# Kernel tuning notes

Measured on AMD Instinct MI355X. Metric: run time of the kernel, lower is better.

## Reference

```python
import jax, jax.numpy as jnp
import numpy as np

# Standard SMPL kinematic tree (child -> parent); root's entry unused.
PARENTS = np.array([0, 0, 0, 0, 1, 2, 3, 4, 5, 6, 7, 8, 9, 9, 9, 12, 13, 14, 16, 17, 18, 19, 20, 21], dtype=np.int32)
N_JOINTS = 24


def _rodrigues(r):
    # r: [..., 3] axis-angle -> [..., 3, 3] rotation matrices.
    # Original adds N(0,1e-8) noise to avoid div-by-zero; we use a deterministic eps.
    theta = jnp.linalg.norm(r, axis=-1, keepdims=True) + 1e-8
    rh = r / theta
    cos = jnp.cos(theta)[..., None]
    sin = jnp.sin(theta)[..., None]
    z = jnp.zeros_like(rh[..., 0])
    K = jnp.stack([z, -rh[..., 2], rh[..., 1],
                   rh[..., 2], z, -rh[..., 0],
                   -rh[..., 1], rh[..., 0], z], axis=-1).reshape(r.shape[:-1] + (3, 3))
    outer = rh[..., :, None] * rh[..., None, :]
    eye = jnp.eye(3, dtype=r.dtype)
    return cos * eye + (1.0 - cos) * outer + sin * K


def setup_inputs() -> dict:
    key = jax.random.key(0)
    ks = jax.random.split(key, 7)
    N, V, J, B = 512, 6890, 24, 10
    beta = jax.random.normal(ks[0], (N, B), dtype=jnp.float32)
    pose = jax.random.normal(ks[1], (N, J * 3), dtype=jnp.float32)
    v_template = jax.random.normal(ks[2], (V, 3), dtype=jnp.float32)
    shapedirs = jax.random.normal(ks[3], (V, 3, B), dtype=jnp.float32) * 0.03
    posedirs = jax.random.normal(ks[4], (V, 3, (J - 1) * 9), dtype=jnp.float32) * 0.01
    J_regressor = jax.random.uniform(ks[5], (J, V), dtype=jnp.float32)
    J_regressor = J_regressor / jnp.sum(J_regressor, axis=1, keepdims=True)  # NonNegUnitSum(axis=1)
    weights = jax.random.uniform(ks[6], (V, J), dtype=jnp.float32)
    weights = weights / jnp.sum(weights, axis=1, keepdims=True)  # NonNegUnitSum(axis=1)
    return {"beta": beta, "pose": pose, "v_template": v_template, "shapedirs": shapedirs,
            "posedirs": posedirs, "J_regressor": J_regressor, "weights": weights}


def reference(beta, pose, v_template, shapedirs, posedirs, J_regressor, weights):
    N = beta.shape[0]
    dt = beta.dtype
    # Shape blendshapes: [N,V,3]
    v_shaped = jnp.einsum('nb,vcb->nvc', beta, shapedirs) + v_template
    # Joint locations: [N,J,3]
    J_loc = jnp.einsum('jv,nvc->njc', J_regressor, v_shaped)
    # Per-joint rotations: [N,24,3,3]
    R = _rodrigues(pose.reshape(N, N_JOINTS, 3))
    # Pose blendshapes
    lrotmin = (R[:, 1:] - jnp.eye(3, dtype=dt)).reshape(N, (N_JOINTS - 1) * 9)
    v_posed = v_shaped + jnp.einsum('np,vcp->nvc', lrotmin, posedirs)
    # Kinematic chain of 4x4 transforms
    bottom = jnp.broadcast_to(jnp.array([0.0, 0.0, 0.0, 1.0], dtype=dt), (N, 1, 4))

    def make_T(Rm, t):  # [N,3,3], [N,3] -> [N,4,4]
        return jnp.concatenate([jnp.concatenate([Rm, t[..., None]], axis=-1), bottom], axis=-2)

    G = [make_T(R[:, 0], J_loc[:, 0])]
    for i in range(1, N_JOINTS):
        p = int(PARENTS[i])
        G.append(jnp.matmul(G[p], make_T(R[:, i], J_loc[:, i] - J_loc[:, p])))
    G = jnp.stack(G, axis=1)  # [N,24,4,4]
    # Remove rest-pose joint translation: G[...,:,3] -= G @ [J,0]
    Jh = jnp.concatenate([J_loc, jnp.zeros_like(J_loc[..., :1])], axis=-1)  # [N,24,4]
    RJ = jnp.einsum('njab,njb->nja', G, Jh)
    G = G - jnp.pad(RJ[..., None], ((0, 0), (0, 0), (0, 0), (3, 0)))
    # Linear blend skinning: per-vertex blended transform [N,V,4,4]
    T = jnp.einsum('njab,vj->nvab', G, weights)
    vh = jnp.concatenate([v_posed, jnp.ones_like(v_posed[..., :1])], axis=-1)  # [N,V,4]
    v = jnp.einsum('nvab,nvb->nva', T, vh)
    return v[..., :3]
```

## Files before the change

kernel.cpp:

```cpp
#include <hip/hip_runtime.h>

#define V_CNT 6890
#define N_B 512
#define NP 207
#define KPAD 224
#define RTOT 20670
#define RPAD 20736
#define PREP_BLKS 2268
#define JS1_BLKS 384
#define W_BLKS 27

typedef unsigned short ushort_t;
typedef __attribute__((ext_vector_type(4))) float f32x4;
typedef __attribute__((ext_vector_type(8))) short s16x8;
typedef __attribute__((ext_vector_type(2))) float f32x2;

#define O_PART 0u
#define O_G2   65536u
#define O_A    655360u
#define O_W    917504u
#define O_B    1441792u
#define O_PB   10747904u

__device__ __constant__ int PAR[24] = {0,0,0,0,1,2,3,4,5,6,7,8,9,9,9,12,13,14,16,17,18,19,20,21};
__device__ __constant__ int LVL[36] = {
    1, 2, 3,-1,   4, 5, 6,-1,   7, 8, 9,-1,
   10,11,12,13,  14,-1,-1,-1,  15,16,17,-1,
   18,19,-1,-1,  20,21,-1,-1,  22,23,-1,-1};

__device__ __forceinline__ ushort_t f2bf(float f) {
    union { float f; unsigned u; } x; x.f = f;
    unsigned u = x.u + 0x7fffu + ((x.u >> 16) & 1u);
    return (ushort_t)(u >> 16);
}
__device__ __forceinline__ float bf2f(ushort_t h) {
    union { unsigned u; float f; } x; x.u = ((unsigned)h) << 16;
    return x.f;
}

__global__ __launch_bounds__(256) void k_pre(const float* __restrict__ pdirs,
                                             const float* __restrict__ sdirs,
                                             const float* __restrict__ vtemp,
                                             const float* __restrict__ jreg,
                                             const float* __restrict__ wts,
                                             ushort_t* __restrict__ Bm,
                                             float* __restrict__ part,
                                             ushort_t* __restrict__ Wp) {
    int b = blockIdx.x;
    int tid = threadIdx.x;
    if (b < PREP_BLKS) {
        int g = b * 256 + tid;
        int r = g / 28;
        int k0 = (g - r * 28) * 8;
        s16x8 pk;
        if (r < RTOT) {
            const float* pr = pdirs + (size_t)r * NP;
            const float* sr = sdirs + (size_t)r * 10;
#pragma unroll
            for (int i = 0; i < 8; i++) {
                int k = k0 + i;
                float v = 0.f;
                if (k < NP) v = pr[k];
                else if (k < 217) v = sr[k - NP];
                pk[i] = (short)f2bf(v);
            }
        } else {
#pragma unroll
            for (int i = 0; i < 8; i++) pk[i] = 0;
        }
        *(s16x8*)(Bm + (size_t)r * KPAD + k0) = pk;
    } else if (b < PREP_BLKS + JS1_BLKS) {
        int b2 = b - PREP_BLKS;
        int ch = b2 & 15;
        int j = b2 >> 4;
        int v0 = ch * 432;
        int vend = v0 + 432; if (vend > V_CNT) vend = V_CNT;
        float acc[33];
#pragma unroll
        for (int i = 0; i < 33; i++) acc[i] = 0.f;
        for (int v = v0 + tid; v < vend; v += 256) {
            float r = jreg[j * V_CNT + v];
            const float* sd = sdirs + v * 30;
#pragma unroll
            for (int i = 0; i < 30; i++) acc[i] += r * sd[i];
            acc[30] += r * vtemp[v * 3 + 0];
            acc[31] += r * vtemp[v * 3 + 1];
            acc[32] += r * vtemp[v * 3 + 2];
        }
#pragma unroll
        for (int off = 32; off > 0; off >>= 1) {
#pragma unroll
            for (int i = 0; i < 33; i++) acc[i] += __shfl_down(acc[i], off);
        }
        __shared__ float red[4][33];
        int w = tid >> 6, lane = tid & 63;
        if (lane == 0) {
#pragma unroll
            for (int i = 0; i < 33; i++) red[w][i] = acc[i];
        }
        __syncthreads();
        if (tid < 33) {
            float s = red[0][tid] + red[1][tid] + red[2][tid] + red[3][tid];
            part[b2 * 33 + tid] = s;
        }
    } else {
        int v = (b - PREP_BLKS - JS1_BLKS) * 256 + tid;
        ushort_t o[32];
        if (v < V_CNT) {
            const float* wr = wts + v * 24;
#pragma unroll
            for (int j = 0; j < 24; j++) o[j] = f2bf(wr[j]);
        } else {
#pragma unroll
            for (int j = 0; j < 24; j++) o[j] = 0;
        }
#pragma unroll
        for (int j = 24; j < 32; j++) o[j] = 0;
#pragma unroll
        for (int q = 0; q < 4; q++)
            *(s16x8*)(Wp + (size_t)v * 32 + q * 8) = *(s16x8*)&o[q * 8];
    }
}

__global__ __launch_bounds__(128) void k_chain(const float* __restrict__ beta,
                                               const float* __restrict__ pose,
                                               const float* __restrict__ part,
                                               ushort_t* __restrict__ G2,
                                               ushort_t* __restrict__ Am) {
    __shared__ float JSl[720];
    __shared__ float JTl[72];
    __shared__ float Rl[2][24][9];
    __shared__ float Jl[2][24][3];
    __shared__ float Tm[2][24][16];
    __shared__ float G[2][24][16];
    __shared__ float Gp[2][24][12];
    int tid = threadIdx.x;

    for (int t = tid; t < 792; t += 128) {
        int j = t / 33, i = t - j * 33;
        float s = 0.f;
#pragma unroll
        for (int c = 0; c < 16; c++) s += part[(j * 16 + c) * 33 + i];
        if (i < 30) JSl[j * 30 + i] = s;
        else        JTl[j * 3 + (i - 30)] = s;
    }
    __syncthreads();

    int sub = tid >> 6, lane = tid & 63;
    int n = blockIdx.x * 2 + sub;

    if (lane < 24) {
        int t = lane;
        float x = pose[n * 72 + t * 3 + 0];
        float y = pose[n * 72 + t * 3 + 1];
        float z = pose[n * 72 + t * 3 + 2];
        float th = sqrtf(x * x + y * y + z * z) + 1e-8f;
        float inv = 1.f / th;
        float rx = x * inv, ry = y * inv, rz = z * inv;
        float c = cosf(th), s = sinf(th), omc = 1.f - c;
        Rl[sub][t][0] = c + omc * rx * rx;
        Rl[sub][t][1] = omc * rx * ry - s * rz;
        Rl[sub][t][2] = omc * rx * rz + s * ry;
        Rl[sub][t][3] = omc * ry * rx + s * rz;
        Rl[sub][t][4] = c + omc * ry * ry;
        Rl[sub][t][5] = omc * ry * rz - s * rx;
        Rl[sub][t][6] = omc * rz * rx - s * ry;
        Rl[sub][t][7] = omc * rz * ry + s * rx;
        Rl[sub][t][8] = c + omc * rz * rz;
#pragma unroll
        for (int cc = 0; cc < 3; cc++) {
            float a = JTl[t * 3 + cc];
#pragma unroll
            for (int b = 0; b < 10; b++) a += beta[n * 10 + b] * JSl[(t * 3 + cc) * 10 + b];
            Jl[sub][t][cc] = a;
        }
    }
    __syncthreads();
    if (lane < 24) {
        int t = lane;
        int p = PAR[t];
        float tx, ty, tz;
        if (t == 0) { tx = Jl[sub][0][0]; ty = Jl[sub][0][1]; tz = Jl[sub][0][2]; }
        else { tx = Jl[sub][t][0] - Jl[sub][p][0]; ty = Jl[sub][t][1] - Jl[sub][p][1]; tz = Jl[sub][t][2] - Jl[sub][p][2]; }
        Tm[sub][t][0] = Rl[sub][t][0]; Tm[sub][t][1] = Rl[sub][t][1]; Tm[sub][t][2]  = Rl[sub][t][2]; Tm[sub][t][3]  = tx;
        Tm[sub][t][4] = Rl[sub][t][3]; Tm[sub][t][5] = Rl[sub][t][4]; Tm[sub][t][6]  = Rl[sub][t][5]; Tm[sub][t][7]  = ty;
        Tm[sub][t][8] = Rl[sub][t][6]; Tm[sub][t][9] = Rl[sub][t][7]; Tm[sub][t][10] = Rl[sub][t][8]; Tm[sub][t][11] = tz;
        Tm[sub][t][12] = 0.f; Tm[sub][t][13] = 0.f; Tm[sub][t][14] = 0.f; Tm[sub][t][15] = 1.f;
    }
    __syncthreads();
    if (lane < 16) G[sub][0][lane] = Tm[sub][0][lane];
    __syncthreads();
#pragma unroll
    for (int p9 = 0; p9 < 9; p9++) {
        int slot = lane >> 4, el = lane & 15;
        int j = LVL[p9 * 4 + slot];
        if (j >= 0) {
            int par = PAR[j];
            int a = el >> 2, bb = el & 3;
            float s = G[sub][par][a * 4 + 0] * Tm[sub][j][0 * 4 + bb]
                    + G[sub][par][a * 4 + 1] * Tm[sub][j][1 * 4 + bb]
                    + G[sub][par][a * 4 + 2] * Tm[sub][j][2 * 4 + bb]
                    + G[sub][par][a * 4 + 3] * Tm[sub][j][3 * 4 + bb];
            G[sub][j][el] = s;
        }
        __syncthreads();
    }
    if (lane < 24) {
        int t = lane;
        float jx = Jl[sub][t][0], jy = Jl[sub][t][1], jz = Jl[sub][t][2];
#pragma unroll
        for (int a = 0; a < 3; a++) {
            float g0 = G[sub][t][a * 4 + 0], g1 = G[sub][t][a * 4 + 1];
            float g2 = G[sub][t][a * 4 + 2], g3 = G[sub][t][a * 4 + 3];
            Gp[sub][t][a * 4 + 0] = g0;
            Gp[sub][t][a * 4 + 1] = g1;
            Gp[sub][t][a * 4 + 2] = g2;
            Gp[sub][t][a * 4 + 3] = g3 - (g0 * jx + g1 * jy + g2 * jz);
        }
    }
    __syncthreads();
    {
        int quad = lane >> 4, lm = lane & 15;
        s16x8 pk;
#pragma unroll
        for (int jj = 0; jj < 8; jj++) {
            int joint = quad * 8 + jj;
            float val = (joint < 24 && lm < 12) ? Gp[sub][joint][lm] : 0.f;
            pk[jj] = (short)f2bf(val);
        }
        *(s16x8*)(G2 + (size_t)n * 512 + lane * 8) = pk;
    }
    for (int idx = lane; idx < KPAD; idx += 64) {
        float val;
        if (idx < NP) {
            int j = 1 + idx / 9;
            int e = idx - (j - 1) * 9;
            float d = (e == 0 || e == 4 || e == 8) ? 1.f : 0.f;
            val = Rl[sub][j][e] - d;
        } else if (idx < 217) {
            val = beta[n * 10 + (idx - NP)];
        } else val = 0.f;
        Am[n * KPAD + idx] = f2bf(val);
    }
}

__global__ __launch_bounds__(256) void k_gemm(const ushort_t* __restrict__ A,
                                              const ushort_t* __restrict__ B,
                                              const float* __restrict__ vtemp,
                                              ushort_t* __restrict__ C) {
    __shared__ __align__(16) ushort_t a_lds[128 * 40];
    __shared__ __align__(16) ushort_t b_lds[128 * 40];
    int tid = threadIdx.x;
    int rblk = blockIdx.x * 128;
    int n0 = blockIdx.y * 128;
    int w = tid >> 6, lane = tid & 63;
    int quad = lane >> 4, lm = lane & 15;
    int m0w = (w >> 1) * 64, r0w = (w & 1) * 64;

    f32x4 acc[4][4];
#pragma unroll
    for (int a = 0; a < 4; a++)
#pragma unroll
        for (int b = 0; b < 4; b++) acc[a][b] = (f32x4)0.f;

    int srow = tid >> 1, koff = (tid & 1) * 16;
    const ushort_t* ag = A + (size_t)(n0 + srow) * KPAD + koff;
    const ushort_t* bg = B + (size_t)(rblk + srow) * KPAD + koff;

#pragma unroll 1
    for (int kc = 0; kc < 7; kc++) {
        s16x8 av0 = *(const s16x8*)(ag + kc * 32);
        s16x8 av1 = *(const s16x8*)(ag + kc * 32 + 8);
        s16x8 bv0 = *(const s16x8*)(bg + kc * 32);
        s16x8 bv1 = *(const s16x8*)(bg + kc * 32 + 8);
        __syncthreads();
        *(s16x8*)&a_lds[srow * 40 + koff] = av0;
        *(s16x8*)&a_lds[srow * 40 + koff + 8] = av1;
        *(s16x8*)&b_lds[srow * 40 + koff] = bv0;
        *(s16x8*)&b_lds[srow * 40 + koff + 8] = bv1;
        __syncthreads();
        s16x8 af[4], bf[4];
#pragma unroll
        for (int mt = 0; mt < 4; mt++)
            af[mt] = *(const s16x8*)&a_lds[(m0w + mt * 16 + lm) * 40 + quad * 8];
#pragma unroll
        for (int rt = 0; rt < 4; rt++)
            bf[rt] = *(const s16x8*)&b_lds[(r0w + rt * 16 + lm) * 40 + quad * 8];
#pragma unroll
        for (int mt = 0; mt < 4; mt++)
#pragma unroll
            for (int rt = 0; rt < 4; rt++)
                acc[mt][rt] = __builtin_amdgcn_mfma_f32_16x16x32_bf16(af[mt], bf[rt], acc[mt][rt], 0, 0, 0);
    }
#pragma unroll
    for (int mt = 0; mt < 4; mt++) {
#pragma unroll
        for (int rt = 0; rt < 4; rt++) {
            int col = rblk + r0w + rt * 16 + lm;
            float vt = (col < RTOT) ? vtemp[col] : 0.f;
#pragma unroll
            for (int i = 0; i < 4; i++) {
                int row = n0 + m0w + mt * 16 + quad * 4 + i;
                C[(size_t)row * RPAD + col] = f2bf(acc[mt][rt][i] + vt);
            }
        }
    }
}

__global__ __launch_bounds__(256) void k_lbs(const ushort_t* __restrict__ Wp,
                                             const ushort_t* __restrict__ G2,
                                             const ushort_t* __restrict__ pb,
                                             float* __restrict__ out) {
    __shared__ float T[4][64][19];
    __shared__ float ost[4][192];
    int tid = threadIdx.x, w = tid >> 6, lane = tid & 63;
    int quad = lane >> 4, lm = lane & 15;
    int v0 = blockIdx.x * 256;
    int n = blockIdx.y * 4 + w;

    s16x8 bfr = *(const s16x8*)(G2 + (size_t)n * 512 + lane * 8);
    const ushort_t* pbn = pb + (size_t)n * RPAD;

#pragma unroll 1
    for (int s = 0; s < 4; s++) {
        int vs = v0 + s * 64;
        const ushort_t* pp = pbn + (vs + lane) * 3;
        float px = bf2f(pp[0]), py = bf2f(pp[1]), pz = bf2f(pp[2]);

        f32x4 acc[4];
#pragma unroll
        for (int mt = 0; mt < 4; mt++) {
            s16x8 af = *(const s16x8*)(Wp + (size_t)(vs + mt * 16 + lm) * 32 + quad * 8);
            acc[mt] = __builtin_amdgcn_mfma_f32_16x16x32_bf16(af, bfr, (f32x4)0.f, 0, 0, 0);
        }
#pragma unroll
        for (int mt = 0; mt < 4; mt++)
#pragma unroll
            for (int i = 0; i < 4; i++)
                T[w][mt * 16 + quad * 4 + i][lm] = acc[mt][i];

        const float* Tr = &T[w][lane][0];
        float o0 = Tr[3]  + Tr[0] * px + Tr[1] * py + Tr[2]  * pz;
        float o1 = Tr[7]  + Tr[4] * px + Tr[5] * py + Tr[6]  * pz;
        float o2 = Tr[11] + Tr[8] * px + Tr[9] * py + Tr[10] * pz;
        ost[w][lane * 3 + 0] = o0;
        ost[w][lane * 3 + 1] = o1;
        ost[w][lane * 3 + 2] = o2;

        int cnt = V_CNT - vs; if (cnt > 64) cnt = 64;
        if (cnt > 0) {
            int nh = (cnt * 3) >> 1;
            float* obase = out + ((size_t)n * V_CNT + vs) * 3;
            for (int j2 = lane; j2 < nh; j2 += 64)
                *(f32x2*)(obase + j2 * 2) = *(const f32x2*)&ost[w][j2 * 2];
        }
    }
}

extern "C" void kernel_launch(void* const* d_in, const int* in_sizes, int n_in,
                              void* d_out, int out_size, void* d_ws, size_t ws_size,
                              hipStream_t stream) {
    const float* beta  = (const float*)d_in[0];
    const float* pose  = (const float*)d_in[1];
    const float* vtemp = (const float*)d_in[2];
    const float* sdirs = (const float*)d_in[3];
    const float* pdirs = (const float*)d_in[4];
    const float* jreg  = (const float*)d_in[5];
    const float* wts   = (const float*)d_in[6];
    char* ws = (char*)d_ws;
    float*    ws_part = (float*)(ws + O_PART);
    ushort_t* ws_G2   = (ushort_t*)(ws + O_G2);
    ushort_t* ws_A    = (ushort_t*)(ws + O_A);
    ushort_t* ws_W    = (ushort_t*)(ws + O_W);
    ushort_t* ws_B    = (ushort_t*)(ws + O_B);
    ushort_t* ws_pb   = (ushort_t*)(ws + O_PB);
    float* out = (float*)d_out;

    k_pre<<<dim3(PREP_BLKS + JS1_BLKS + W_BLKS), dim3(256), 0, stream>>>(
        pdirs, sdirs, vtemp, jreg, wts, ws_B, ws_part, ws_W);
    k_chain<<<dim3(N_B / 2), dim3(128), 0, stream>>>(beta, pose, ws_part, ws_G2, ws_A);
    k_gemm<<<dim3(RPAD / 128, N_B / 128), dim3(256), 0, stream>>>(ws_A, ws_B, vtemp, ws_pb);
    k_lbs<<<dim3(27, N_B / 4), dim3(256), 0, stream>>>(ws_W, ws_G2, ws_pb, out);
}
```

Measured before the change: 148.1 us.

## Fuse blendshape GEMM with skinning and pre-swizzle operands into MFMA fragment layout

The separate GEMM kernel that wrote posed vertices to a bf16 global buffer and the skinning kernel that read them back are merged into one kernel. Each wave keeps its GEMM tile in LDS and applies the blended joint transforms directly. A and B are pre-swizzled into MFMA fragment order so the GEMM loads fragments straight from global with register double-buffering and no LDS staging. This removes a roughly 21 MB intermediate round trip and one launch, at the cost of higher register and LDS use per block and more, smaller blocks. The joint-regressor partial reduction is also halved to 8 chunks.

New measurement: 142.0 us. 1.04x faster.

```diff
diff --git a/kernel.cpp b/kernel.cpp
--- a/kernel.cpp
+++ b/kernel.cpp
@@ -7,7 +7,7 @@
 #define RTOT 20670
 #define RPAD 20736
 #define PREP_BLKS 2268
-#define JS1_BLKS 384
+#define JS1_BLKS 192
 #define W_BLKS 27
 
 typedef unsigned short ushort_t;
@@ -20,7 +20,6 @@
 #define O_A    655360u
 #define O_W    917504u
 #define O_B    1441792u
-#define O_PB   10747904u
 
 __device__ __constant__ int PAR[24] = {0,0,0,0,1,2,3,4,5,6,7,8,9,9,9,12,13,14,16,17,18,19,20,21};
 __device__ __constant__ int LVL[36] = {
@@ -43,15 +42,20 @@
                                              const float* __restrict__ vtemp,
                                              const float* __restrict__ jreg,
                                              const float* __restrict__ wts,
-                                             ushort_t* __restrict__ Bm,
+                                             ushort_t* __restrict__ Bswz,
                                              float* __restrict__ part,
                                              ushort_t* __restrict__ Wp) {
     int b = blockIdx.x;
     int tid = threadIdx.x;
     if (b < PREP_BLKS) {
         int g = b * 256 + tid;
-        int r = g / 28;
-        int k0 = (g - r * 28) * 8;
+        int rtile = g / 448;
+        int rem = g - rtile * 448;
+        int kc = rem >> 6;
+        int lane = rem & 63;
+        int quad = lane >> 4, lm = lane & 15;
+        int r = rtile * 16 + lm;
+        int k0 = kc * 32 + quad * 8;
         s16x8 pk;
         if (r < RTOT) {
             const float* pr = pdirs + (size_t)r * NP;
@@ -68,13 +72,13 @@
 #pragma unroll
             for (int i = 0; i < 8; i++) pk[i] = 0;
         }
-        *(s16x8*)(Bm + (size_t)r * KPAD + k0) = pk;
+        *(s16x8*)(Bswz + (size_t)g * 8) = pk;
     } else if (b < PREP_BLKS + JS1_BLKS) {
         int b2 = b - PREP_BLKS;
-        int ch = b2 & 15;
-        int j = b2 >> 4;
-        int v0 = ch * 432;
-        int vend = v0 + 432; if (vend > V_CNT) vend = V_CNT;
+        int ch = b2 & 7;
+        int j = b2 >> 3;
+        int v0 = ch * 862;
+        int vend = v0 + 862; if (vend > V_CNT) vend = V_CNT;
         float acc[33];
 #pragma unroll
         for (int i = 0; i < 33; i++) acc[i] = 0.f;
@@ -126,7 +130,7 @@
                                                const float* __restrict__ pose,
                                                const float* __restrict__ part,
                                                ushort_t* __restrict__ G2,
-                                               ushort_t* __restrict__ Am) {
+                                               ushort_t* __restrict__ Aswz) {
     __shared__ float JSl[720];
     __shared__ float JTl[72];
     __shared__ float Rl[2][24][9];
@@ -140,7 +144,7 @@
         int j = t / 33, i = t - j * 33;
         float s = 0.f;
 #pragma unroll
-        for (int c = 0; c < 16; c++) s += part[(j * 16 + c) * 33 + i];
+        for (int c = 0; c < 8; c++) s += part[(j * 8 + c) * 33 + i];
         if (i < 30) JSl[j * 30 + i] = s;
         else        JTl[j * 3 + (i - 30)] = s;
     }
@@ -230,129 +234,138 @@
         }
         *(s16x8*)(G2 + (size_t)n * 512 + lane * 8) = pk;
     }
-    for (int idx = lane; idx < KPAD; idx += 64) {
-        float val;
-        if (idx < NP) {
-            int j = 1 + idx / 9;
-            int e = idx - (j - 1) * 9;
-            float d = (e == 0 || e == 4 || e == 8) ? 1.f : 0.f;
-            val = Rl[sub][j][e] - d;
-        } else if (idx < 217) {
-            val = beta[n * 10 + (idx - NP)];
-        } else val = 0.f;
-        Am[n * KPAD + idx] = f2bf(val);
-    }
-}
-
-__global__ __launch_bounds__(256) void k_gemm(const ushort_t* __restrict__ A,
-                                              const ushort_t* __restrict__ B,
-                                              const float* __restrict__ vtemp,
-                                              ushort_t* __restrict__ C) {
-    __shared__ __align__(16) ushort_t a_lds[128 * 40];
-    __shared__ __align__(16) ushort_t b_lds[128 * 40];
-    int tid = threadIdx.x;
-    int rblk = blockIdx.x * 128;
-    int n0 = blockIdx.y * 128;
-    int w = tid >> 6, lane = tid & 63;
-    int quad = lane >> 4, lm = lane & 15;
-    int m0w = (w >> 1) * 64, r0w = (w & 1) * 64;
-
-    f32x4 acc[4][4];
-#pragma unroll
-    for (int a = 0; a < 4; a++)
-#pragma unroll
-        for (int b = 0; b < 4; b++) acc[a][b] = (f32x4)0.f;
-
-    int srow = tid >> 1, koff = (tid & 1) * 16;
-    const ushort_t* ag = A + (size_t)(n0 + srow) * KPAD + koff;
-    const ushort_t* bg = B + (size_t)(rblk + srow) * KPAD + koff;
-
-#pragma unroll 1
-    for (int kc = 0; kc < 7; kc++) {
-        s16x8 av0 = *(const s16x8*)(ag + kc * 32);
-        s16x8 av1 = *(const s16x8*)(ag + kc * 32 + 8);
-        s16x8 bv0 = *(const s16x8*)(bg + kc * 32);
-        s16x8 bv1 = *(const s16x8*)(bg + kc * 32 + 8);
-        __syncthreads();
-        *(s16x8*)&a_lds[srow * 40 + koff] = av0;
-        *(s16x8*)&a_lds[srow * 40 + koff + 8] = av1;
-        *(s16x8*)&b_lds[srow * 40 + koff] = bv0;
-        *(s16x8*)&b_lds[srow * 40 + koff + 8] = bv1;
-        __syncthreads();
-        s16x8 af[4], bf[4];
-#pragma unroll
-        for (int mt = 0; mt < 4; mt++)
-            af[mt] = *(const s16x8*)&a_lds[(m0w + mt * 16 + lm) * 40 + quad * 8];
-#pragma unroll
-        for (int rt = 0; rt < 4; rt++)
-            bf[rt] = *(const s16x8*)&b_lds[(r0w + rt * 16 + lm) * 40 + quad * 8];
-#pragma unroll
-        for (int mt = 0; mt < 4; mt++)
-#pragma unroll
-            for (int rt = 0; rt < 4; rt++)
-                acc[mt][rt] = __builtin_amdgcn_mfma_f32_16x16x32_bf16(af[mt], bf[rt], acc[mt][rt], 0, 0, 0);
-    }
-#pragma unroll
-    for (int mt = 0; mt < 4; mt++) {
-#pragma unroll
-        for (int rt = 0; rt < 4; rt++) {
-            int col = rblk + r0w + rt * 16 + lm;
-            float vt = (col < RTOT) ? vtemp[col] : 0.f;
-#pragma unroll
-            for (int i = 0; i < 4; i++) {
-                int row = n0 + m0w + mt * 16 + quad * 4 + i;
-                C[(size_t)row * RPAD + col] = f2bf(acc[mt][rt][i] + vt);
-            }
-        }
-    }
-}
-
-__global__ __launch_bounds__(256) void k_lbs(const ushort_t* __restrict__ Wp,
-                                             const ushort_t* __restrict__ G2,
-                                             const ushort_t* __restrict__ pb,
-                                             float* __restrict__ out) {
-    __shared__ float T[4][64][19];
-    __shared__ float ost[4][192];
+    if (lane < 28) {
+        int kc = lane >> 2, quad2 = lane & 3;
+        s16x8 pk;
+#pragma unroll
+        for (int j = 0; j < 8; j++) {
+            int k = kc * 32 + quad2 * 8 + j;
+            float val;
+            if (k < NP) {
+                int jo = 1 + k / 9;
+                int e = k - (jo - 1) * 9;
+                float d = (e == 0 || e == 4 || e == 8) ? 1.f : 0.f;
+                val = Rl[sub][jo][e] - d;
+            } else if (k < 217) {
+                val = beta[n * 10 + (k - NP)];
+            } else val = 0.f;
+            pk[j] = (short)f2bf(val);
+        }
+        *(s16x8*)(Aswz + (((size_t)(n >> 4) * 7 + kc) * 64 + (quad2 * 16 + (n & 15))) * 8) = pk;
+    }
+}
+
+__global__ __launch_bounds__(256) void k_fused(const ushort_t* __restrict__ Aswz,
+                                               const ushort_t* __restrict__ Bswz,
+                                               const ushort_t* __restrict__ Wp,
+                                               const ushort_t* __restrict__ G2,
+                                               const float* __restrict__ vtemp,
+                                               float* __restrict__ out) {
+    __shared__ ushort_t vp[4][96][34];
+    __shared__ float Tl[4][2][32][19];
+    __shared__ float ost[4][2][96];
     int tid = threadIdx.x, w = tid >> 6, lane = tid & 63;
     int quad = lane >> 4, lm = lane & 15;
-    int v0 = blockIdx.x * 256;
-    int n = blockIdx.y * 4 + w;
-
-    s16x8 bfr = *(const s16x8*)(G2 + (size_t)n * 512 + lane * 8);
-    const ushort_t* pbn = pb + (size_t)n * RPAD;
+    int rh = w & 1, nh = w >> 1;
+    int n_w = blockIdx.y * 64 + nh * 32;
+    int vs_w = blockIdx.x * 64 + rh * 32;
+    int rtile0 = blockIdx.x * 12 + rh * 6;
+    int ntile0 = blockIdx.y * 4 + nh * 2;
+
+    f32x4 acc[2][6];
+#pragma unroll
+    for (int a = 0; a < 2; a++)
+#pragma unroll
+        for (int b = 0; b < 6; b++) acc[a][b] = (f32x4)0.f;
+
+    s16x8 af[2][2], bf[2][6];
+#pragma unroll
+    for (int mt = 0; mt < 2; mt++)
+        af[0][mt] = *(const s16x8*)(Aswz + ((size_t)(ntile0 + mt) * 7 + 0) * 512 + lane * 8);
+#pragma unroll
+    for (int rt = 0; rt < 6; rt++)
+        bf[0][rt] = *(const s16x8*)(Bswz + ((size_t)(rtile0 + rt) * 7 + 0) * 512 + lane * 8);
+#pragma unroll
+    for (int kc = 0; kc < 7; kc++) {
+        int cur = kc & 1, nxt = cur ^ 1;
+        if (kc < 6) {
+#pragma unroll
+            for (int mt = 0; mt < 2; mt++)
+                af[nxt][mt] = *(const s16x8*)(Aswz + ((size_t)(ntile0 + mt) * 7 + kc + 1) * 512 + lane * 8);
+#pragma unroll
+            for (int rt = 0; rt < 6; rt++)
+                bf[nxt][rt] = *(const s16x8*)(Bswz + ((size_t)(rtile0 + rt) * 7 + kc + 1) * 512 + lane * 8);
+        }
+#pragma unroll
+        for (int mt = 0; mt < 2; mt++)
+#pragma unroll
+            for (int rt = 0; rt < 6; rt++)
+                acc[mt][rt] = __builtin_amdgcn_mfma_f32_16x16x32_bf16(af[cur][mt], bf[cur][rt], acc[mt][rt], 0, 0, 0);
+    }
+
+    float vt[6];
+#pragma unroll
+    for (int rt = 0; rt < 6; rt++) {
+        int col = blockIdx.x * 192 + rh * 96 + rt * 16 + lm;
+        vt[rt] = (col < RTOT) ? vtemp[col] : 0.f;
+    }
+#pragma unroll
+    for (int mt = 0; mt < 2; mt++) {
+#pragma unroll
+        for (int rt = 0; rt < 6; rt++) {
+            int rl = rt * 16 + lm;
+            int nl0 = mt * 16 + quad * 4;
+            unsigned d0 = (unsigned)f2bf(acc[mt][rt][0] + vt[rt]) | ((unsigned)f2bf(acc[mt][rt][1] + vt[rt]) << 16);
+            unsigned d1 = (unsigned)f2bf(acc[mt][rt][2] + vt[rt]) | ((unsigned)f2bf(acc[mt][rt][3] + vt[rt]) << 16);
+            *(unsigned*)&vp[w][rl][nl0]     = d0;
+            *(unsigned*)&vp[w][rl][nl0 + 2] = d1;
+        }
+    }
+
+    s16x8 wf[2];
+#pragma unroll
+    for (int mt = 0; mt < 2; mt++)
+        wf[mt] = *(const s16x8*)(Wp + (size_t)(vs_w + mt * 16 + lm) * 32 + quad * 8);
+
+    int sub = lane >> 5, vl = lane & 31;
+    int rem = V_CNT - vs_w;
+    int nfl = rem >= 32 ? 96 : rem * 3;
+    int nh2 = nfl >> 1;
 
 #pragma unroll 1
-    for (int s = 0; s < 4; s++) {
-        int vs = v0 + s * 64;
-        const ushort_t* pp = pbn + (vs + lane) * 3;
-        float px = bf2f(pp[0]), py = bf2f(pp[1]), pz = bf2f(pp[2]);
-
-        f32x4 acc[4];
-#pragma unroll
-        for (int mt = 0; mt < 4; mt++) {
-            s16x8 af = *(const s16x8*)(Wp + (size_t)(vs + mt * 16 + lm) * 32 + quad * 8);
-            acc[mt] = __builtin_amdgcn_mfma_f32_16x16x32_bf16(af, bfr, (f32x4)0.f, 0, 0, 0);
-        }
-#pragma unroll
-        for (int mt = 0; mt < 4; mt++)
-#pragma unroll
-            for (int i = 0; i < 4; i++)
-                T[w][mt * 16 + quad * 4 + i][lm] = acc[mt][i];
-
-        const float* Tr = &T[w][lane][0];
-        float o0 = Tr[3]  + Tr[0] * px + Tr[1] * py + Tr[2]  * pz;
-        float o1 = Tr[7]  + Tr[4] * px + Tr[5] * py + Tr[6]  * pz;
-        float o2 = Tr[11] + Tr[8] * px + Tr[9] * py + Tr[10] * pz;
-        ost[w][lane * 3 + 0] = o0;
-        ost[w][lane * 3 + 1] = o1;
-        ost[w][lane * 3 + 2] = o2;
-
-        int cnt = V_CNT - vs; if (cnt > 64) cnt = 64;
-        if (cnt > 0) {
-            int nh = (cnt * 3) >> 1;
-            float* obase = out + ((size_t)n * V_CNT + vs) * 3;
-            for (int j2 = lane; j2 < nh; j2 += 64)
-                *(f32x2*)(obase + j2 * 2) = *(const f32x2*)&ost[w][j2 * 2];
+    for (int t = 0; t < 16; t++) {
+        int na = n_w + 2 * t;
+        s16x8 ga = *(const s16x8*)(G2 + (size_t)na * 512 + lane * 8);
+        s16x8 gb = *(const s16x8*)(G2 + (size_t)(na + 1) * 512 + lane * 8);
+        f32x4 ta[2], tb[2];
+#pragma unroll
+        for (int mt = 0; mt < 2; mt++) {
+            ta[mt] = __builtin_amdgcn_mfma_f32_16x16x32_bf16(wf[mt], ga, (f32x4)0.f, 0, 0, 0);
+            tb[mt] = __builtin_amdgcn_mfma_f32_16x16x32_bf16(wf[mt], gb, (f32x4)0.f, 0, 0, 0);
+        }
+#pragma unroll
+        for (int mt = 0; mt < 2; mt++)
+#pragma unroll
+            for (int i = 0; i < 4; i++) {
+                Tl[w][0][mt * 16 + quad * 4 + i][lm] = ta[mt][i];
+                Tl[w][1][mt * 16 + quad * 4 + i][lm] = tb[mt][i];
+            }
+        const float* Tr = &Tl[w][sub][vl][0];
+        const ushort_t* pr0 = &vp[w][vl * 3 + 0][2 * t + sub];
+        const ushort_t* pr1 = &vp[w][vl * 3 + 1][2 * t + sub];
+        const ushort_t* pr2 = &vp[w][vl * 3 + 2][2 * t + sub];
+        float p0 = bf2f(*pr0), p1 = bf2f(*pr1), p2 = bf2f(*pr2);
+        float o0 = Tr[3]  + Tr[0] * p0 + Tr[1] * p1 + Tr[2]  * p2;
+        float o1 = Tr[7]  + Tr[4] * p0 + Tr[5] * p1 + Tr[6]  * p2;
+        float o2 = Tr[11] + Tr[8] * p0 + Tr[9] * p1 + Tr[10] * p2;
+        ost[w][sub][vl * 3 + 0] = o0;
+        ost[w][sub][vl * 3 + 1] = o1;
+        ost[w][sub][vl * 3 + 2] = o2;
+#pragma unroll
+        for (int s2 = 0; s2 < 2; s2++) {
+            float* ob = out + ((size_t)(na + s2) * V_CNT + vs_w) * 3;
+            if (lane < nh2)
+                *(f32x2*)(ob + lane * 2) = *(const f32x2*)&ost[w][s2][lane * 2];
         }
     }
 }
@@ -373,12 +386,10 @@
     ushort_t* ws_A    = (ushort_t*)(ws + O_A);
     ushort_t* ws_W    = (ushort_t*)(ws + O_W);
     ushort_t* ws_B    = (ushort_t*)(ws + O_B);
-    ushort_t* ws_pb   = (ushort_t*)(ws + O_PB);
     float* out = (float*)d_out;
 
     k_pre<<<dim3(PREP_BLKS + JS1_BLKS + W_BLKS), dim3(256), 0, stream>>>(
         pdirs, sdirs, vtemp, jreg, wts, ws_B, ws_part, ws_W);
     k_chain<<<dim3(N_B / 2), dim3(128), 0, stream>>>(beta, pose, ws_part, ws_G2, ws_A);
-    k_gemm<<<dim3(RPAD / 128, N_B / 128), dim3(256), 0, stream>>>(ws_A, ws_B, vtemp, ws_pb);
-    k_lbs<<<dim3(27, N_B / 4), dim3(256), 0, stream>>>(ws_W, ws_G2, ws_pb, out);
-}
+    k_fused<<<dim3(108, N_B / 64), dim3(256), 0, stream>>>(ws_A, ws_B, ws_W, ws_G2, vtemp, out);
+}
```
